# Performance work log

Hardware: AMD Instinct MI355X
Metric: run time of the kernel (lower is better)

Reference implementation:

```python
import jax, jax.numpy as jnp
import numpy as np

B, S, SR, H, NH, L, V, FF = 4, 512, 512, 1024, 16, 6, 32000, 4096
HD = H // NH  # 64
PAD = 2


def setup_inputs() -> dict:
    key = jax.random.key(0)
    ks = jax.random.split(key, 40)
    f32 = jnp.float32

    def n(k, shape, scale=0.02):
        return jax.random.normal(k, shape, f32) * scale

    encoder_outputs = jax.random.normal(ks[0], (B, SR, H), f32)
    decoder_input = jax.random.randint(ks[1], (B, S), 0, V)
    decoder_input = jnp.where(decoder_input == PAD, 3, decoder_input)
    decoder_input = decoder_input.at[:, S - 64:].set(PAD).at[:, 0].set(5)
    encoder_input = jax.random.randint(ks[2], (B, SR), 0, V)
    encoder_input = jnp.where(encoder_input == PAD, 3, encoder_input)
    encoder_input = encoder_input.at[:, SR - 64:].set(PAD)

    emb = jax.random.normal(ks[3], (V, H), f32).at[PAD].set(0.0)  # padding_idx=2 row is zero

    return {
        'encoder_outputs': encoder_outputs,
        'decoder_input': decoder_input,
        'encoder_input': encoder_input,
        'emb': emb,
        'wq1': n(ks[4], (L, H, H)), 'bq1': jnp.zeros((L, H), f32),
        'wk1': n(ks[5], (L, H, H)), 'bk1': jnp.zeros((L, H), f32),
        'wv1': n(ks[6], (L, H, H)), 'bv1': jnp.zeros((L, H), f32),
        'wo1': n(ks[7], (L, H, H)), 'bo1': jnp.zeros((L, H), f32),
        'pos1': jax.random.normal(ks[8], (L, 2 * S - 1, HD), f32),  # torch.randn init
        'wq2': n(ks[9], (L, H, H)), 'bq2': jnp.zeros((L, H), f32),
        'wk2': n(ks[10], (L, H, H)), 'bk2': jnp.zeros((L, H), f32),
        'wv2': n(ks[11], (L, H, H)), 'bv2': jnp.zeros((L, H), f32),
        'wo2': n(ks[12], (L, H, H)), 'bo2': jnp.zeros((L, H), f32),
        'ln1g': jnp.ones((L, H), f32), 'ln1b': jnp.zeros((L, H), f32),
        'ln2g': jnp.ones((L, H), f32), 'ln2b': jnp.zeros((L, H), f32),
        'ln3g': jnp.ones((L, H), f32), 'ln3b': jnp.zeros((L, H), f32),
        'wf1': n(ks[13], (L, H, FF)), 'bf1': jnp.zeros((L, FF), f32),
        'wf2': n(ks[14], (L, FF, H)), 'bf2': jnp.zeros((L, H), f32),
        'wout': n(ks[15], (H, V)), 'bout': jnp.zeros((V,), f32),
    }


def _split_heads(x):
    b, l, _ = x.shape
    return x.reshape(b, l, NH, HD).transpose(0, 2, 1, 3)  # b h l d


def _layer_norm(x, g, b):
    m = x.mean(-1, keepdims=True)
    v = ((x - m) ** 2).mean(-1, keepdims=True)
    return (x - m) / jnp.sqrt(v + 1e-5) * g + b


def _skew(q, P):
    # Transformer-XL style relative-position skew. q: [b,h,S,d] (already scaled), P: [2S-1,d]
    b = q.shape[0]
    pe = jnp.einsum('bhid,jd->bhij', q, P)                 # [b,h,S,2S-1]
    pe = jnp.pad(pe, ((0, 0), (0, 0), (0, 0), (0, 1)))      # [b,h,S,2S]
    pe = pe.reshape(b, NH, 2 * S * S)
    pe = jnp.pad(pe, ((0, 0), (0, 0), (0, S - 1)))
    pe = pe.reshape(b, NH, S + 1, 2 * S - 1)
    return pe[:, :, :-1, -S:]                               # [b,h,S,S]


def _attention(xq, xkv, wq, bq, wk, bk, wv, bv, wo, bo, pos, add_mask, causal):
    b = xq.shape[0]
    q = _split_heads(xq @ wq + bq) / np.float32(np.sqrt(HD))
    k = _split_heads(xkv @ wk + bk)
    v = _split_heads(xkv @ wv + bv)
    att = jnp.einsum('bhid,bhjd->bhij', q, k)
    if pos is not None:
        att = att + _skew(q, pos)
    if causal:
        i = jnp.arange(S)[:, None]
        j = jnp.arange(att.shape[-1])[None, :]
        att = jnp.where(j > i, -jnp.inf, att)
    if add_mask is not None:
        att = att + add_mask
    s = jax.nn.softmax(att, axis=-1)
    o = jnp.einsum('bhqk,bhkd->bhqd', s, v)
    o = o.transpose(0, 2, 1, 3).reshape(b, S, H)
    return o @ wo + bo


def _forward(encoder_outputs, decoder_input, encoder_input, emb,
             wq1, bq1, wk1, bk1, wv1, bv1, wo1, bo1, pos1,
             wq2, bq2, wk2, bk2, wv2, bv2, wo2, bo2,
             ln1g, ln1b, ln2g, ln2b, ln3g, ln3b,
             wf1, bf1, wf2, bf2, wout, bout):
    self_mask = jnp.where(decoder_input == PAD, -jnp.inf, 0.0)[:, None, None, :]   # [b,1,1,S]
    cross_mask = jnp.where(encoder_input == PAD, -jnp.inf, 0.0)[:, None, None, :]  # [b,1,1,SR]
    x = emb[decoder_input]  # dropout_p=0 -> identity
    for i in range(L):
        a1 = _attention(x, x, wq1[i], bq1[i], wk1[i], bk1[i], wv1[i], bv1[i],
                        wo1[i], bo1[i], pos1[i], self_mask, True)
        x1 = _layer_norm(a1 + x, ln1g[i], ln1b[i])
        a2 = _attention(x1, encoder_outputs, wq2[i], bq2[i], wk2[i], bk2[i], wv2[i], bv2[i],
                        wo2[i], bo2[i], None, cross_mask, False)
        x2 = _layer_norm(a2 + x1, ln2g[i], ln2b[i])
        ff = jax.nn.relu(x2 @ wf1[i] + bf1[i]) @ wf2[i] + bf2[i]
        x = _layer_norm(ff + x2, ln3g[i], ln3b[i])
    return jax.nn.log_softmax(x @ wout + bout, axis=-1)  # [b,S,V]


def reference(encoder_outputs, decoder_input, encoder_input, emb,
              wq1, bq1, wk1, bk1, wv1, bv1, wo1, bo1, pos1,
              wq2, bq2, wk2, bk2, wv2, bv2, wo2, bo2,
              ln1g, ln1b, ln2g, ln2b, ln3g, ln3b,
              wf1, bf1, wf2, bf2, wout, bout):
    return _forward(encoder_outputs, decoder_input, encoder_input, emb,
                    wq1, bq1, wk1, bk1, wv1, bv1, wo1, bo1, pos1,
                    wq2, bq2, wk2, bk2, wv2, bv2, wo2, bo2,
                    ln1g, ln1b, ln2g, ln2b, ln3g, ln3b,
                    wf1, bf1, wf2, bf2, wout, bout)
```

## Files before the change

kernel.cpp:

```cpp
#include <hip/hip_runtime.h>


typedef unsigned short u16;
typedef short s16x8 __attribute__((ext_vector_type(8)));
typedef unsigned short u16x4 __attribute__((ext_vector_type(4)));
typedef unsigned short u16x8 __attribute__((ext_vector_type(8)));
typedef float f32x4 __attribute__((ext_vector_type(4)));

#define PADTOK 2
#define NEG_INF (-__builtin_inff())

static __device__ __forceinline__ u16 f2bf(float f) {
  unsigned u = __float_as_uint(f);
  u += 0x7fffu + ((u >> 16) & 1u);
  return (u16)(u >> 16);
}
static __device__ __forceinline__ float bf2f(u16 h) {
  return __uint_as_float(((unsigned)h) << 16);
}
static __device__ __forceinline__ float f16tof(u16 h) {
  _Float16 x = __builtin_bit_cast(_Float16, h);
  return (float)x;
}
static __device__ __forceinline__ u16 ftof16(float v) {
  _Float16 x = (_Float16)v;
  return __builtin_bit_cast(u16, x);
}
static __device__ __forceinline__ f32x4 mfma16(s16x8 a, s16x8 b, f32x4 c) {
  asm("v_mfma_f32_16x16x32_bf16 %0, %1, %2, %0" : "+v"(c) : "v"(a), "v"(b));
  return c;
}
static __device__ __forceinline__ void gll16(const void* g, void* l) {
  __builtin_amdgcn_global_load_lds((const __attribute__((address_space(1))) void*)g,
                                   (__attribute__((address_space(3))) void*)l, 16, 0, 0);
}
static __device__ __forceinline__ size_t hsidx(int m, int n) {
  return ((size_t)((m >> 9) * 16 + (n >> 6))) * 32768u + (size_t)(m & 511) * 64u + (size_t)(n & 63);
}
static __device__ __forceinline__ size_t vtidx(int m, int n) {
  return ((size_t)((m >> 9) * 16 + (n >> 6))) * 65536u + (size_t)(n & 63) * 512u + (size_t)(m & 511);
}

static __device__ __forceinline__ void raster2(int& bm, int& bn, int GM0) {
  const int nm = gridDim.y, nn = gridDim.x;
  int bid = blockIdx.y * nn + blockIdx.x;
  const int nwg = nm * nn;
  const int q = nwg >> 3, r = nwg & 7;
  const int x = bid & 7, p = bid >> 3;
  bid = (x < r ? x * (q + 1) : r * (q + 1) + (x - r) * q) + p;
  const int GM = nm < GM0 ? nm : GM0;
  const int pg = GM * nn;
  const int gi = bid / pg, rem = bid - gi * pg;
  const int left = nm - gi * GM;
  const int gm = left < GM ? left : GM;
  bm = gi * GM + rem % gm;
  bn = rem / gm;
}

template<int EPI, bool BF16OUT, int MFR, bool RELU, bool RESID, int SKIP, int GMT>
__global__ __launch_bounds__(256)
void bgemm(const u16* __restrict__ A, long long sAg,
           const u16* __restrict__ Bt, long long sBg,
           const float* __restrict__ bias, const float* __restrict__ bias2,
           const float* __restrict__ bias3,
           const float* __restrict__ Res,
           void* __restrict__ Cv, u16* __restrict__ C2, u16* __restrict__ C3,
           long long sCg, int ldc, int K, float scale)
{
  constexpr int BM = MFR * 32;
  __shared__ u16 As[BM * 64];
  __shared__ u16 Bs[128 * 64];
  int bmi, bni;
  raster2(bmi, bni, GMT);
  const int bm0 = bmi * BM, bn0 = bni * 128;
  if constexpr (SKIP == 1) {
    if (bn0 > bm0 + BM - 1) return;
  }
  if constexpr (SKIP == 2) {
    if ((bm0 & 511) + bn0 <= 256) return;
  }
  const int g = blockIdx.z;
  const u16* Ag = A + (size_t)g * (size_t)sAg;
  const u16* Bg = Bt + (size_t)g * (size_t)sBg;
  const int tid = threadIdx.x, l = tid & 63, w = tid >> 6;
  const int wm = w >> 1, wn = w & 1;
  const int rsel = l & 15, kg = l >> 4, xs = l & 7;

  f32x4 acc[MFR][4];
#pragma unroll
  for (int i = 0; i < MFR; ++i)
#pragma unroll
    for (int j = 0; j < 4; ++j) acc[i][j] = (f32x4){0.f, 0.f, 0.f, 0.f};

  const int srow = l >> 3;
  const int sch  = (l & 7) ^ srow;
  const u16* Agp = Ag + ((size_t)(bm0 + w * 8 * MFR + srow)) * (size_t)K + sch * 8;
  const u16* Bgp = Bg + ((size_t)(bn0 + w * 32 + srow)) * (size_t)K + sch * 8;
  char* AsL = (char*)As + (w * 8 * MFR) * 128;
  char* BsL = (char*)Bs + (w * 32) * 128;

  for (int k0 = 0; k0 < K; k0 += 64) {
    __syncthreads();
#pragma unroll
    for (int i = 0; i < MFR; ++i)
      gll16(Agp + (size_t)i * 8 * K + k0, AsL + i * 1024);
#pragma unroll
    for (int i = 0; i < 4; ++i)
      gll16(Bgp + (size_t)i * 8 * K + k0, BsL + i * 1024);
    __syncthreads();

    const int arow0 = (wm * (MFR * 16) + rsel) * 128;
    const int brow0 = (wn * 64 + rsel) * 128;
#pragma unroll
    for (int ks = 0; ks < 2; ++ks) {
      const int ch = ((ks * 4 + kg) ^ xs) * 16;
      s16x8 af[MFR], bfr[4];
#pragma unroll
      for (int mf = 0; mf < MFR; ++mf)
        af[mf] = *(const s16x8*)((const char*)As + arow0 + mf * 2048 + ch);
#pragma unroll
      for (int nf = 0; nf < 4; ++nf)
        bfr[nf] = *(const s16x8*)((const char*)Bs + brow0 + nf * 2048 + ch);
#pragma unroll
      for (int mf = 0; mf < MFR; ++mf)
#pragma unroll
        for (int nf = 0; nf < 4; ++nf)
          acc[mf][nf] = mfma16(af[mf], bfr[nf], acc[mf][nf]);
    }
  }

#pragma unroll
  for (int mf = 0; mf < MFR; ++mf) {
#pragma unroll
    for (int nf = 0; nf < 4; ++nf) {
      const int n = bn0 + wn * 64 + nf * 16 + rsel;
      int sub = 0, nl = n;
      const float* bp = bias;
      if constexpr (EPI == 4) {
        sub = n >> 10; nl = n & 1023;
        bp = (sub == 0) ? bias : (sub == 1) ? bias2 : bias3;
      }
      if constexpr (EPI == 5) {
        sub = n >> 10; nl = n & 1023;
        bp = (sub == 0) ? bias : bias2;
      }
      const float bv = bp ? bp[nl] : 0.f;
      float sc = 1.f;
      if constexpr (EPI == 0 || EPI == 1) sc = scale;
      if constexpr (EPI == 4) sc = (sub == 0) ? scale : 1.f;
#pragma unroll
      for (int e = 0; e < 4; ++e) {
        const int m = bm0 + wm * (MFR * 16) + mf * 16 + kg * 4 + e;
        float v = (acc[mf][nf][e] + bv) * sc;
        if constexpr (RELU) v = fmaxf(v, 0.f);
        if constexpr (RESID) v += Res[(size_t)m * (size_t)ldc + n];
        if constexpr (EPI == 0) {
          const size_t idx = (size_t)g * (size_t)sCg + (size_t)m * (size_t)ldc + n;
          if constexpr (BF16OUT) ((u16*)Cv)[idx] = f2bf(v);
          else                   ((float*)Cv)[idx] = v;
        } else if constexpr (EPI == 1) {
          ((u16*)Cv)[hsidx(m, nl)] = f2bf(v);
        } else if constexpr (EPI == 4) {
          if (sub == 2)      C3[vtidx(m, nl)] = f2bf(v);
          else if (sub == 1) C2[hsidx(m, nl)] = f2bf(v);
          else               ((u16*)Cv)[hsidx(m, nl)] = f2bf(v);
        } else if constexpr (EPI == 5) {
          if (sub == 0) ((u16*)Cv)[hsidx(m, nl)] = f2bf(v);
          else          C2[vtidx(m, nl)] = f2bf(v);
        } else if constexpr (EPI == 6) {
          ((u16*)Cv)[(size_t)m * (size_t)ldc + n] = ftof16(v);
        }
      }
    }
  }
}

template<bool SELF>
__global__ __launch_bounds__(256)
void fused_attn(const u16* __restrict__ Qb, const u16* __restrict__ Kb,
                const u16* __restrict__ Vt, const u16* __restrict__ PE,
                const float* __restrict__ maskf, u16* __restrict__ O)
{
  __shared__ u16 SP[32][520];
  __shared__ float Of[4][32][68];
  __shared__ float rs[32];
  const int it = blockIdx.x, g = blockIdx.y, b = g >> 4, h = g & 15;
  const int i0 = it * 32;
  const int CT = SELF ? (i0 + 32) : 512;
  const int tid = threadIdx.x, l = tid & 63, w = tid >> 6;
  const int rsel = l & 15, kg = l >> 4;

  const u16* Qg = Qb + (size_t)g * 32768u;
  const u16* Kg = Kb + (size_t)g * 32768u;
  const u16* Vg = Vt + (size_t)g * 65536u;

  s16x8 qf[2][2];
#pragma unroll
  for (int rt = 0; rt < 2; ++rt)
#pragma unroll
    for (int ks = 0; ks < 2; ++ks)
      qf[rt][ks] = *(const s16x8*)(Qg + (size_t)(i0 + rt * 16 + rsel) * 64u + ks * 32 + kg * 8);

  for (int ct = w; ct * 16 < CT; ct += 4) {
    const int j = ct * 16 + rsel;
    const s16x8 kf0 = *(const s16x8*)(Kg + (size_t)j * 64u + kg * 8);
    const s16x8 kf1 = *(const s16x8*)(Kg + (size_t)j * 64u + 32 + kg * 8);
    f32x4 a0 = {0.f, 0.f, 0.f, 0.f}, a1 = {0.f, 0.f, 0.f, 0.f};
    a0 = mfma16(qf[0][0], kf0, a0);
    a0 = mfma16(qf[0][1], kf1, a0);
    a1 = mfma16(qf[1][0], kf0, a1);
    a1 = mfma16(qf[1][1], kf1, a1);
    const float mj = maskf[b * 512 + j];
#pragma unroll
    for (int rt = 0; rt < 2; ++rt) {
      const f32x4 av = rt ? a1 : a0;
#pragma unroll
      for (int e = 0; e < 4; ++e) {
        const int r = rt * 16 + kg * 4 + e;
        float v = av[e] + mj;
        if constexpr (SELF) {
          const int i = i0 + r;
          if (j > i) v = NEG_INF;
          else       v += bf2f(PE[((size_t)(g * 512 + i)) * 512u + (511 + j - i)]);
        }
        SP[r][j] = f2bf(v);
      }
    }
  }
  __syncthreads();

  const int r = tid >> 3, sc0 = (tid & 7) * 4;
  float mx = NEG_INF;
  for (int c = sc0; c < CT; c += 32) {
    const u16x4 h4 = *(const u16x4*)&SP[r][c];
#pragma unroll
    for (int e = 0; e < 4; ++e) mx = fmaxf(mx, bf2f(h4[e]));
  }
#pragma unroll
  for (int o = 1; o < 8; o <<= 1) mx = fmaxf(mx, __shfl_xor(mx, o, 64));
  float sum = 0.f;
  for (int c = sc0; c < CT; c += 32) {
    const u16x4 h4 = *(const u16x4*)&SP[r][c];
    const float p0 = expf(bf2f(h4[0]) - mx), p1 = expf(bf2f(h4[1]) - mx);
    const float p2 = expf(bf2f(h4[2]) - mx), p3 = expf(bf2f(h4[3]) - mx);
    sum += p0 + p1 + p2 + p3;
    const u16x4 o4 = {f2bf(p0), f2bf(p1), f2bf(p2), f2bf(p3)};
    *(u16x4*)&SP[r][c] = o4;
  }
#pragma unroll
  for (int o = 1; o < 8; o <<= 1) sum += __shfl_xor(sum, o, 64);
  if ((tid & 7) == 0) rs[r] = 1.f / sum;
  __syncthreads();

  f32x4 oa[2][4];
#pragma unroll
  for (int rt = 0; rt < 2; ++rt)
#pragma unroll
    for (int nt = 0; nt < 4; ++nt) oa[rt][nt] = (f32x4){0.f, 0.f, 0.f, 0.f};
  const int nk = CT >> 5;
  for (int kt = w; kt < nk; kt += 4) {
    const s16x8 pf0 = *(const s16x8*)&SP[rsel][kt * 32 + kg * 8];
    const s16x8 pf1 = *(const s16x8*)&SP[16 + rsel][kt * 32 + kg * 8];
    s16x8 vf[4];
#pragma unroll
    for (int nt = 0; nt < 4; ++nt)
      vf[nt] = *(const s16x8*)(Vg + (size_t)(nt * 16 + rsel) * 512u + kt * 32 + kg * 8);
#pragma unroll
    for (int nt = 0; nt < 4; ++nt) {
      oa[0][nt] = mfma16(pf0, vf[nt], oa[0][nt]);
      oa[1][nt] = mfma16(pf1, vf[nt], oa[1][nt]);
    }
  }
#pragma unroll
  for (int rt = 0; rt < 2; ++rt)
#pragma unroll
    for (int nt = 0; nt < 4; ++nt)
#pragma unroll
      for (int e = 0; e < 4; ++e)
        Of[w][rt * 16 + kg * 4 + e][nt * 16 + rsel] = oa[rt][nt][e];
  __syncthreads();

  const int c0 = (tid & 7) * 8;
  const float inv = rs[r];
  float ov[8];
#pragma unroll
  for (int q = 0; q < 2; ++q) {
    const float4 s0 = *(const float4*)&Of[0][r][c0 + q * 4];
    const float4 s1 = *(const float4*)&Of[1][r][c0 + q * 4];
    const float4 s2 = *(const float4*)&Of[2][r][c0 + q * 4];
    const float4 s3 = *(const float4*)&Of[3][r][c0 + q * 4];
    ov[q * 4 + 0] = (s0.x + s1.x + s2.x + s3.x) * inv;
    ov[q * 4 + 1] = (s0.y + s1.y + s2.y + s3.y) * inv;
    ov[q * 4 + 2] = (s0.z + s1.z + s2.z + s3.z) * inv;
    ov[q * 4 + 3] = (s0.w + s1.w + s2.w + s3.w) * inv;
  }
  const u16x8 o8 = {f2bf(ov[0]), f2bf(ov[1]), f2bf(ov[2]), f2bf(ov[3]),
                    f2bf(ov[4]), f2bf(ov[5]), f2bf(ov[6]), f2bf(ov[7])};
  *(u16x8*)(O + ((size_t)(b * 512 + i0 + r)) * 1024u + h * 64 + c0) = o8;
}

static __device__ __forceinline__ void tconv_tile(const float* in, int N,
                                                  u16* out, int K, int k0, int n0) {
  __shared__ u16 L[64][72];
  const int t = threadIdx.x;
  const int rk = t >> 4, cn = (t & 15) * 4;
#pragma unroll
  for (int q = 0; q < 4; ++q) {
    const int kk = k0 + rk + q * 16;
    float4 v = *(const float4*)(in + (size_t)kk * (size_t)N + n0 + cn);
    L[cn + 0][rk + q * 16] = f2bf(v.x);
    L[cn + 1][rk + q * 16] = f2bf(v.y);
    L[cn + 2][rk + q * 16] = f2bf(v.z);
    L[cn + 3][rk + q * 16] = f2bf(v.w);
  }
  __syncthreads();
  const int rn = t >> 2, ck = (t & 3) * 16;
  u16* op = out + (size_t)(n0 + rn) * (size_t)K + k0 + ck;
  *(s16x8*)op       = *(const s16x8*)&L[rn][ck];
  *(s16x8*)(op + 8) = *(const s16x8*)&L[rn][ck + 8];
}

__global__ __launch_bounds__(256)
void conv_layer(const float* w0, const float* w1, const float* w2, const float* w3,
                const float* w4, const float* w5, const float* w6, const float* w7,
                const float* w8, const float* w9, u16* WT) {
  const int b = blockIdx.x;
  const float* in; u16* out; int N, K, kt, nt;
  if (b < 2048) {
    const int j = b >> 8, t = b & 255;
    const float* ws[8] = {w0, w1, w2, w3, w4, w5, w6, w7};
    in = ws[j]; out = WT + (size_t)j * 1048576u; K = 1024; N = 1024;
    kt = t >> 4; nt = t & 15;
  } else if (b < 3072) {
    const int t = b - 2048;
    in = w8; out = WT + 8388608u; K = 1024; N = 4096; kt = t >> 6; nt = t & 63;
  } else {
    const int t = b - 3072;
    in = w9; out = WT + 12582912u; K = 4096; N = 1024; kt = t >> 4; nt = t & 15;
  }
  tconv_tile(in, N, out, K, kt * 64, nt * 64);
}

__global__ __launch_bounds__(256)
void conv_wout(const float* in, u16* out) {
  const int b = blockIdx.x;
  const int kt = b / 500, nt = b % 500;
  tconv_tile(in, 32000, out, 1024, kt * 64, nt * 64);
}

__global__ void conv_bf16(const float* __restrict__ in, u16* __restrict__ out) {
  const int i = (blockIdx.x * 256 + threadIdx.x) * 4;
  float4 v = *(const float4*)(in + i);
  u16x4 h = {f2bf(v.x), f2bf(v.y), f2bf(v.z), f2bf(v.w)};
  *(u16x4*)(out + i) = h;
}

__global__ void conv_pos(const float* __restrict__ pos, u16* __restrict__ posb) {
  const int idx = (blockIdx.x * 256 + threadIdx.x) * 4;
  const int lyr = idx >> 15, rem = idx & 32767;
  float4 v = *(const float4*)(pos + (size_t)lyr * 65472u + rem);
  u16x4 h = {f2bf(v.x), f2bf(v.y), f2bf(v.z), f2bf(v.w)};
  *(u16x4*)(posb + idx) = h;
}

__global__ void mask_kernel(const int* __restrict__ dec, const int* __restrict__ enc,
                            float* __restrict__ mD, float* __restrict__ mE) {
  const int i = blockIdx.x * 256 + threadIdx.x;
  mD[i] = (dec[i] == PADTOK) ? NEG_INF : 0.f;
  mE[i] = (enc[i] == PADTOK) ? NEG_INF : 0.f;
}

static __device__ __forceinline__ float wred_sum(float v) {
#pragma unroll
  for (int o = 32; o > 0; o >>= 1) v += __shfl_down(v, o, 64);
  return v;
}
static __device__ __forceinline__ float wred_max(float v) {
#pragma unroll
  for (int o = 32; o > 0; o >>= 1) v = fmaxf(v, __shfl_down(v, o, 64));
  return v;
}
static __device__ __forceinline__ float bred_sum(float v, float* sm) {
  const int lane = threadIdx.x & 63, wid = threadIdx.x >> 6;
  v = wred_sum(v);
  if (lane == 0) sm[wid] = v;
  __syncthreads();
  if (threadIdx.x == 0) sm[0] = sm[0] + sm[1] + sm[2] + sm[3];
  __syncthreads();
  const float r = sm[0];
  __syncthreads();
  return r;
}

__global__ void embed_kernel(const int* __restrict__ dec, const float* __restrict__ emb,
                             float* __restrict__ X, u16* __restrict__ Xh) {
  const int m = blockIdx.x, t = threadIdx.x;
  const int tok = dec[m];
  float4 v = ((const float4*)(emb + (size_t)tok * 1024u))[t];
  ((float4*)(X + (size_t)m * 1024u))[t] = v;
  u16x4 h = {f2bf(v.x), f2bf(v.y), f2bf(v.z), f2bf(v.w)};
  *(u16x4*)(Xh + (size_t)m * 1024u + t * 4) = h;
}

__global__ void layernorm_kernel(const float* __restrict__ R,
                                 const float* __restrict__ gw, const float* __restrict__ bw,
                                 float* __restrict__ Y, u16* __restrict__ Yh) {
  __shared__ float sm[4];
  const int m = blockIdx.x, t = threadIdx.x;
  float4 v = ((const float4*)(R + (size_t)m * 1024u))[t];
  float s = v.x + v.y + v.z + v.w;
  s = bred_sum(s, sm);
  const float mean = s * (1.f / 1024.f);
  const float d0 = v.x - mean, d1 = v.y - mean, d2 = v.z - mean, d3 = v.w - mean;
  float q = d0 * d0 + d1 * d1 + d2 * d2 + d3 * d3;
  q = bred_sum(q, sm);
  const float rstd = rsqrtf(q * (1.f / 1024.f) + 1e-5f);
  const int c = t * 4;
  float4 o;
  o.x = d0 * rstd * gw[c + 0] + bw[c + 0];
  o.y = d1 * rstd * gw[c + 1] + bw[c + 1];
  o.z = d2 * rstd * gw[c + 2] + bw[c + 2];
  o.w = d3 * rstd * gw[c + 3] + bw[c + 3];
  ((float4*)(Y + (size_t)m * 1024u))[t] = o;
  u16x4 h = {f2bf(o.x), f2bf(o.y), f2bf(o.z), f2bf(o.w)};
  *(u16x4*)(Yh + (size_t)m * 1024u + c) = h;
}

__global__ __launch_bounds__(512)
void log_softmax_kernel(float* __restrict__ out) {
  __shared__ u16 row[32000];
  __shared__ float sm[8];
  const int m = blockIdx.x, tid = threadIdx.x;
  const u16* src = (const u16*)out + (size_t)m * 64000u;
  for (int c = tid; c < 4000; c += 512)
    *(u16x8*)&row[c * 8] = *(const u16x8*)(src + c * 8);
  __syncthreads();
  float mx = NEG_INF;
  for (int c = tid; c < 4000; c += 512) {
    const u16x8 h = *(const u16x8*)&row[c * 8];
#pragma unroll
    for (int e = 0; e < 8; ++e) mx = fmaxf(mx, f16tof(h[e]));
  }
  mx = wred_max(mx);
  if ((tid & 63) == 0) sm[tid >> 6] = mx;
  __syncthreads();
  if (tid == 0) {
    float a = sm[0];
#pragma unroll
    for (int wI = 1; wI < 8; ++wI) a = fmaxf(a, sm[wI]);
    sm[0] = a;
  }
  __syncthreads();
  mx = sm[0];
  __syncthreads();
  float s = 0.f;
  for (int c = tid; c < 4000; c += 512) {
    const u16x8 h = *(const u16x8*)&row[c * 8];
#pragma unroll
    for (int e = 0; e < 8; ++e) s += expf(f16tof(h[e]) - mx);
  }
  s = wred_sum(s);
  if ((tid & 63) == 0) sm[tid >> 6] = s;
  __syncthreads();
  if (tid == 0) {
    float a = 0.f;
#pragma unroll
    for (int wI = 0; wI < 8; ++wI) a += sm[wI];
    sm[0] = a;
  }
  __syncthreads();
  const float lse = mx + logf(sm[0]);
  float* dst = out + (size_t)m * 32000u;
  for (int c = tid; c < 4000; c += 512) {
    const u16x8 h = *(const u16x8*)&row[c * 8];
    float4 o0, o1;
    o0.x = f16tof(h[0]) - lse; o0.y = f16tof(h[1]) - lse;
    o0.z = f16tof(h[2]) - lse; o0.w = f16tof(h[3]) - lse;
    o1.x = f16tof(h[4]) - lse; o1.y = f16tof(h[5]) - lse;
    o1.z = f16tof(h[6]) - lse; o1.w = f16tof(h[7]) - lse;
    ((float4*)dst)[c * 2]     = o0;
    ((float4*)dst)[c * 2 + 1] = o1;
  }
}

extern "C" void kernel_launch(void* const* d_in, const int* in_sizes, int n_in,
                              void* d_out, int out_size, void* d_ws, size_t ws_size,
                              hipStream_t stream) {
  const float* enc_out = (const float*)d_in[0];
  const int*   dec_in  = (const int*)d_in[1];
  const int*   enc_in  = (const int*)d_in[2];
  const float* emb     = (const float*)d_in[3];
  const float* wq1 = (const float*)d_in[4];  const float* bq1 = (const float*)d_in[5];
  const float* wk1 = (const float*)d_in[6];  const float* bk1 = (const float*)d_in[7];
  const float* wv1 = (const float*)d_in[8];  const float* bv1 = (const float*)d_in[9];
  const float* wo1 = (const float*)d_in[10]; const float* bo1 = (const float*)d_in[11];
  const float* pos1 = (const float*)d_in[12];
  const float* wq2 = (const float*)d_in[13]; const float* bq2 = (const float*)d_in[14];
  const float* wk2 = (const float*)d_in[15]; const float* bk2 = (const float*)d_in[16];
  const float* wv2 = (const float*)d_in[17]; const float* bv2 = (const float*)d_in[18];
  const float* wo2 = (const float*)d_in[19]; const float* bo2 = (const float*)d_in[20];
  const float* ln1g = (const float*)d_in[21]; const float* ln1b = (const float*)d_in[22];
  const float* ln2g = (const float*)d_in[23]; const float* ln2b = (const float*)d_in[24];
  const float* ln3g = (const float*)d_in[25]; const float* ln3b = (const float*)d_in[26];
  const float* wf1 = (const float*)d_in[27]; const float* bf1 = (const float*)d_in[28];
  const float* wf2 = (const float*)d_in[29]; const float* bf2 = (const float*)d_in[30];
  const float* wout = (const float*)d_in[31]; const float* bout = (const float*)d_in[32];

  char* ws = (char*)d_ws;
  u16*   WT    = (u16*)(ws + 0);
  float* maskD = (float*)(ws + 33554432);
  float* maskE = (float*)(ws + 33562624);
  u16*   WoutT = (u16*)(ws + 0);
  u16*   PEP   = (u16*)(ws + 67108864);
  float* X     = (float*)(ws + 100663296);
  float* Xa    = (float*)(ws + 109051904);
  float* Xb    = (float*)(ws + 117440512);
  float* Rb    = (float*)(ws + 125829120);
  u16*   Ab16  = (u16*)(ws + 134217728);
  u16*   Q     = (u16*)(ws + 138412032);
  u16*   Kh    = (u16*)(ws + 142606336);
  u16*   VT    = (u16*)(ws + 146800640);
  u16*   Ob16  = (u16*)(ws + 155189248);
  u16*   FFH16 = (u16*)(ws + 159383552);
  u16*   encb  = (u16*)(ws + 176160768);
  u16*   posb  = (u16*)(ws + 180355072);
  float* out   = (float*)d_out;

  embed_kernel<<<2048, 256, 0, stream>>>(dec_in, emb, X, Ab16);
  conv_bf16<<<2048, 256, 0, stream>>>(enc_out, encb);
  conv_pos<<<192, 256, 0, stream>>>(pos1, posb);
  mask_kernel<<<8, 256, 0, stream>>>(dec_in, enc_in, maskD, maskE);

  for (int i = 0; i < 6; ++i) {
    const size_t oHH = (size_t)i * 1048576u, oH = (size_t)i * 1024u;
    const float* bq1i = bq1 + oH; const float* bk1i = bk1 + oH;
    const float* bv1i = bv1 + oH; const float* bo1i = bo1 + oH;
    const float* bq2i = bq2 + oH; const float* bk2i = bk2 + oH;
    const float* bv2i = bv2 + oH; const float* bo2i = bo2 + oH;
    const float* bf1i = bf1 + (size_t)i * 4096u; const float* bf2i = bf2 + oH;
    const u16* posL = posb + (size_t)i * 32768u;

    conv_layer<<<4096, 256, 0, stream>>>(
        wq1 + oHH, wk1 + oHH, wv1 + oHH, wo1 + oHH,
        wq2 + oHH, wk2 + oHH, wv2 + oHH, wo2 + oHH,
        wf1 + (size_t)i * 4194304u, wf2 + (size_t)i * 4194304u, WT);

    bgemm<4, true, 4, false, false, 0, 8><<<dim3(24, 16, 1), 256, 0, stream>>>(
        Ab16, 0, WT, 0, bq1i, bk1i, bv1i, nullptr, Q, Kh, VT, 0, 0, 1024, 0.125f);
    bgemm<0, true, 4, false, false, 2, 8><<<dim3(4, 256, 1), 256, 0, stream>>>(
        Q, 0, posL, 0, nullptr, nullptr, nullptr, nullptr, PEP, nullptr, nullptr,
        0, 512, 64, 1.f);
    fused_attn<true><<<dim3(16, 64), 256, 0, stream>>>(Q, Kh, VT, PEP, maskD, Ob16);
    bgemm<0, false, 2, false, true, 0, 8><<<dim3(8, 32, 1), 256, 0, stream>>>(
        Ob16, 0, WT + 3145728u, 0, bo1i, nullptr, nullptr, X, Rb, nullptr, nullptr,
        0, 1024, 1024, 1.f);
    layernorm_kernel<<<2048, 256, 0, stream>>>(Rb, ln1g + oH, ln1b + oH, Xa, Ab16);

    bgemm<1, true, 2, false, false, 0, 8><<<dim3(8, 32, 1), 256, 0, stream>>>(
        Ab16, 0, WT + 4194304u, 0, bq2i, nullptr, nullptr, nullptr, Q, nullptr, nullptr,
        0, 0, 1024, 0.125f);
    bgemm<5, true, 4, false, false, 0, 8><<<dim3(16, 16, 1), 256, 0, stream>>>(
        encb, 0, WT + 5242880u, 0, bk2i, bv2i, nullptr, nullptr, Kh, VT, nullptr,
        0, 0, 1024, 1.f);
    fused_attn<false><<<dim3(16, 64), 256, 0, stream>>>(Q, Kh, VT, nullptr, maskE, Ob16);
    bgemm<0, false, 2, false, true, 0, 8><<<dim3(8, 32, 1), 256, 0, stream>>>(
        Ob16, 0, WT + 7340032u, 0, bo2i, nullptr, nullptr, Xa, Rb, nullptr, nullptr,
        0, 1024, 1024, 1.f);
    layernorm_kernel<<<2048, 256, 0, stream>>>(Rb, ln2g + oH, ln2b + oH, Xb, Ab16);

    bgemm<0, true, 4, true, false, 0, 8><<<dim3(32, 16, 1), 256, 0, stream>>>(
        Ab16, 0, WT + 8388608u, 0, bf1i, nullptr, nullptr, nullptr, FFH16, nullptr, nullptr,
        0, 4096, 1024, 1.f);
    bgemm<0, false, 2, false, true, 0, 8><<<dim3(8, 32, 1), 256, 0, stream>>>(
        FFH16, 0, WT + 12582912u, 0, bf2i, nullptr, nullptr, Xb, Rb, nullptr, nullptr,
        0, 1024, 4096, 1.f);
    layernorm_kernel<<<2048, 256, 0, stream>>>(Rb, ln3g + oH, ln3b + oH, X, Ab16);
  }

  conv_wout<<<8000, 256, 0, stream>>>(wout, WoutT);
  bgemm<6, false, 4, false, false, 0, 16><<<dim3(250, 16, 1), 256, 0, stream>>>(
      Ab16, 0, WoutT, 0, bout, nullptr, nullptr, nullptr, out, nullptr, nullptr,
      0, 64000, 1024, 1.f);
  log_softmax_kernel<<<2048, 512, 0, stream>>>(out);
}
```

Before: 2.311 ms.

## Give each attention wave its own 16-row query tile and drop block barriers

```diff
diff --git a/kernel.cpp b/kernel.cpp
--- a/kernel.cpp
+++ b/kernel.cpp
@@ -73,9 +73,6 @@
   int bmi, bni;
   raster2(bmi, bni, GMT);
   const int bm0 = bmi * BM, bn0 = bni * 128;
-  if constexpr (SKIP == 1) {
-    if (bn0 > bm0 + BM - 1) return;
-  }
   if constexpr (SKIP == 2) {
     if ((bm0 & 511) + bn0 <= 256) return;
   }
@@ -181,122 +178,98 @@
                 const u16* __restrict__ Vt, const u16* __restrict__ PE,
                 const float* __restrict__ maskf, u16* __restrict__ O)
 {
-  __shared__ u16 SP[32][520];
-  __shared__ float Of[4][32][68];
-  __shared__ float rs[32];
-  const int it = blockIdx.x, g = blockIdx.y, b = g >> 4, h = g & 15;
-  const int i0 = it * 32;
-  const int CT = SELF ? (i0 + 32) : 512;
+  __shared__ u16 SP[4][16][520];
+  __shared__ float rsm[4][16];
+  const int bid = blockIdx.y * 8 + blockIdx.x;
+  const int g = (bid & 7) + 8 * ((bid >> 3) & 7);
+  const int rt = bid >> 6;
+  const int b = g >> 4, h = g & 15;
   const int tid = threadIdx.x, l = tid & 63, w = tid >> 6;
+  const int ti = SELF ? (w * 8 + rt) : (rt * 4 + w);
+  const int i0 = ti * 16;
+  const int CT = SELF ? (i0 + 16) : 512;
   const int rsel = l & 15, kg = l >> 4;
 
   const u16* Qg = Qb + (size_t)g * 32768u;
   const u16* Kg = Kb + (size_t)g * 32768u;
   const u16* Vg = Vt + (size_t)g * 65536u;
-
-  s16x8 qf[2][2];
-#pragma unroll
-  for (int rt = 0; rt < 2; ++rt)
-#pragma unroll
-    for (int ks = 0; ks < 2; ++ks)
-      qf[rt][ks] = *(const s16x8*)(Qg + (size_t)(i0 + rt * 16 + rsel) * 64u + ks * 32 + kg * 8);
-
-  for (int ct = w; ct * 16 < CT; ct += 4) {
-    const int j = ct * 16 + rsel;
-    const s16x8 kf0 = *(const s16x8*)(Kg + (size_t)j * 64u + kg * 8);
-    const s16x8 kf1 = *(const s16x8*)(Kg + (size_t)j * 64u + 32 + kg * 8);
-    f32x4 a0 = {0.f, 0.f, 0.f, 0.f}, a1 = {0.f, 0.f, 0.f, 0.f};
-    a0 = mfma16(qf[0][0], kf0, a0);
-    a0 = mfma16(qf[0][1], kf1, a0);
-    a1 = mfma16(qf[1][0], kf0, a1);
-    a1 = mfma16(qf[1][1], kf1, a1);
-    const float mj = maskf[b * 512 + j];
-#pragma unroll
-    for (int rt = 0; rt < 2; ++rt) {
-      const f32x4 av = rt ? a1 : a0;
-#pragma unroll
-      for (int e = 0; e < 4; ++e) {
-        const int r = rt * 16 + kg * 4 + e;
-        float v = av[e] + mj;
-        if constexpr (SELF) {
-          const int i = i0 + r;
-          if (j > i) v = NEG_INF;
-          else       v += bf2f(PE[((size_t)(g * 512 + i)) * 512u + (511 + j - i)]);
-        }
-        SP[r][j] = f2bf(v);
+  u16 (*sp)[520] = SP[w];
+  float* rs = rsm[w];
+
+  const s16x8 qf0 = *(const s16x8*)(Qg + (size_t)(i0 + rsel) * 64u + kg * 8);
+  const s16x8 qf1 = *(const s16x8*)(Qg + (size_t)(i0 + rsel) * 64u + 32 + kg * 8);
+
+  for (int j0 = 0; j0 < CT; j0 += 16) {
+    const s16x8 kf0 = *(const s16x8*)(Kg + (size_t)(j0 + rsel) * 64u + kg * 8);
+    const s16x8 kf1 = *(const s16x8*)(Kg + (size_t)(j0 + rsel) * 64u + 32 + kg * 8);
+    f32x4 a = {0.f, 0.f, 0.f, 0.f};
+    a = mfma16(qf0, kf0, a);
+    a = mfma16(qf1, kf1, a);
+    const int jj = j0 + rsel;
+    const float mj = maskf[b * 512 + jj];
+#pragma unroll
+    for (int e = 0; e < 4; ++e) {
+      const int r = kg * 4 + e;
+      float v = a[e] + mj;
+      if constexpr (SELF) {
+        const int i = i0 + r;
+        if (jj > i) v = NEG_INF;
+        else        v += bf2f(PE[((size_t)(g * 512 + i)) * 512u + (511 + jj - i)]);
       }
+      sp[r][jj] = f2bf(v);
     }
   }
-  __syncthreads();
-
-  const int r = tid >> 3, sc0 = (tid & 7) * 4;
+  asm volatile("s_waitcnt lgkmcnt(0)" ::: "memory");
+
+  const int sr = l >> 2, sub = l & 3;
   float mx = NEG_INF;
-  for (int c = sc0; c < CT; c += 32) {
-    const u16x4 h4 = *(const u16x4*)&SP[r][c];
+  for (int c = sub * 4; c < CT; c += 16) {
+    const u16x4 h4 = *(const u16x4*)&sp[sr][c];
 #pragma unroll
     for (int e = 0; e < 4; ++e) mx = fmaxf(mx, bf2f(h4[e]));
   }
-#pragma unroll
-  for (int o = 1; o < 8; o <<= 1) mx = fmaxf(mx, __shfl_xor(mx, o, 64));
+  mx = fmaxf(mx, __shfl_xor(mx, 1, 64));
+  mx = fmaxf(mx, __shfl_xor(mx, 2, 64));
   float sum = 0.f;
-  for (int c = sc0; c < CT; c += 32) {
-    const u16x4 h4 = *(const u16x4*)&SP[r][c];
+  for (int c = sub * 4; c < CT; c += 16) {
+    const u16x4 h4 = *(const u16x4*)&sp[sr][c];
     const float p0 = expf(bf2f(h4[0]) - mx), p1 = expf(bf2f(h4[1]) - mx);
     const float p2 = expf(bf2f(h4[2]) - mx), p3 = expf(bf2f(h4[3]) - mx);
     sum += p0 + p1 + p2 + p3;
     const u16x4 o4 = {f2bf(p0), f2bf(p1), f2bf(p2), f2bf(p3)};
-    *(u16x4*)&SP[r][c] = o4;
-  }
-#pragma unroll
-  for (int o = 1; o < 8; o <<= 1) sum += __shfl_xor(sum, o, 64);
-  if ((tid & 7) == 0) rs[r] = 1.f / sum;
-  __syncthreads();
-
-  f32x4 oa[2][4];
-#pragma unroll
-  for (int rt = 0; rt < 2; ++rt)
-#pragma unroll
-    for (int nt = 0; nt < 4; ++nt) oa[rt][nt] = (f32x4){0.f, 0.f, 0.f, 0.f};
-  const int nk = CT >> 5;
-  for (int kt = w; kt < nk; kt += 4) {
-    const s16x8 pf0 = *(const s16x8*)&SP[rsel][kt * 32 + kg * 8];
-    const s16x8 pf1 = *(const s16x8*)&SP[16 + rsel][kt * 32 + kg * 8];
-    s16x8 vf[4];
+    *(u16x4*)&sp[sr][c] = o4;
+  }
+  sum += __shfl_xor(sum, 1, 64);
+  sum += __shfl_xor(sum, 2, 64);
+  if (sub == 0) rs[sr] = 1.f / sum;
+  if (CT & 31) {
+    const u16x4 z = {0, 0, 0, 0};
+    *(u16x4*)&sp[sr][CT + sub * 4] = z;
+  }
+  asm volatile("s_waitcnt lgkmcnt(0)" ::: "memory");
+
+  f32x4 oa[4];
+#pragma unroll
+  for (int nt = 0; nt < 4; ++nt) oa[nt] = (f32x4){0.f, 0.f, 0.f, 0.f};
+  const int nk = (CT + 31) >> 5;
+  for (int kt = 0; kt < nk; ++kt) {
+    const s16x8 pf = *(const s16x8*)&sp[rsel][kt * 32 + kg * 8];
+#pragma unroll
+    for (int nt = 0; nt < 4; ++nt) {
+      const s16x8 vf = *(const s16x8*)(Vg + (size_t)(nt * 16 + rsel) * 512u + kt * 32 + kg * 8);
+      oa[nt] = mfma16(pf, vf, oa[nt]);
+    }
+  }
+
+#pragma unroll
+  for (int e = 0; e < 4; ++e) {
+    const int q = kg * 4 + e;
+    const float inv = rs[q];
+    u16* orow = O + ((size_t)(b * 512 + i0 + q)) * 1024u + h * 64;
 #pragma unroll
     for (int nt = 0; nt < 4; ++nt)
-      vf[nt] = *(const s16x8*)(Vg + (size_t)(nt * 16 + rsel) * 512u + kt * 32 + kg * 8);
-#pragma unroll
-    for (int nt = 0; nt < 4; ++nt) {
-      oa[0][nt] = mfma16(pf0, vf[nt], oa[0][nt]);
-      oa[1][nt] = mfma16(pf1, vf[nt], oa[1][nt]);
-    }
-  }
-#pragma unroll
-  for (int rt = 0; rt < 2; ++rt)
-#pragma unroll
-    for (int nt = 0; nt < 4; ++nt)
-#pragma unroll
-      for (int e = 0; e < 4; ++e)
-        Of[w][rt * 16 + kg * 4 + e][nt * 16 + rsel] = oa[rt][nt][e];
-  __syncthreads();
-
-  const int c0 = (tid & 7) * 8;
-  const float inv = rs[r];
-  float ov[8];
-#pragma unroll
-  for (int q = 0; q < 2; ++q) {
-    const float4 s0 = *(const float4*)&Of[0][r][c0 + q * 4];
-    const float4 s1 = *(const float4*)&Of[1][r][c0 + q * 4];
-    const float4 s2 = *(const float4*)&Of[2][r][c0 + q * 4];
-    const float4 s3 = *(const float4*)&Of[3][r][c0 + q * 4];
-    ov[q * 4 + 0] = (s0.x + s1.x + s2.x + s3.x) * inv;
-    ov[q * 4 + 1] = (s0.y + s1.y + s2.y + s3.y) * inv;
-    ov[q * 4 + 2] = (s0.z + s1.z + s2.z + s3.z) * inv;
-    ov[q * 4 + 3] = (s0.w + s1.w + s2.w + s3.w) * inv;
-  }
-  const u16x8 o8 = {f2bf(ov[0]), f2bf(ov[1]), f2bf(ov[2]), f2bf(ov[3]),
-                    f2bf(ov[4]), f2bf(ov[5]), f2bf(ov[6]), f2bf(ov[7])};
-  *(u16x8*)(O + ((size_t)(b * 512 + i0 + r)) * 1024u + h * 64 + c0) = o8;
+      orow[nt * 16 + rsel] = f2bf(oa[nt][e] * inv);
+  }
 }
 
 static __device__ __forceinline__ void tconv_tile(const float* in, int N,
@@ -550,7 +523,7 @@
     bgemm<0, true, 4, false, false, 2, 8><<<dim3(4, 256, 1), 256, 0, stream>>>(
         Q, 0, posL, 0, nullptr, nullptr, nullptr, nullptr, PEP, nullptr, nullptr,
         0, 512, 64, 1.f);
-    fused_attn<true><<<dim3(16, 64), 256, 0, stream>>>(Q, Kh, VT, PEP, maskD, Ob16);
+    fused_attn<true><<<dim3(8, 64), 256, 0, stream>>>(Q, Kh, VT, PEP, maskD, Ob16);
     bgemm<0, false, 2, false, true, 0, 8><<<dim3(8, 32, 1), 256, 0, stream>>>(
         Ob16, 0, WT + 3145728u, 0, bo1i, nullptr, nullptr, X, Rb, nullptr, nullptr,
         0, 1024, 1024, 1.f);
@@ -562,7 +535,7 @@
     bgemm<5, true, 4, false, false, 0, 8><<<dim3(16, 16, 1), 256, 0, stream>>>(
         encb, 0, WT + 5242880u, 0, bk2i, bv2i, nullptr, nullptr, Kh, VT, nullptr,
         0, 0, 1024, 1.f);
-    fused_attn<false><<<dim3(16, 64), 256, 0, stream>>>(Q, Kh, VT, nullptr, maskE, Ob16);
+    fused_attn<false><<<dim3(8, 64), 256, 0, stream>>>(Q, Kh, VT, nullptr, maskE, Ob16);
     bgemm<0, false, 2, false, true, 0, 8><<<dim3(8, 32, 1), 256, 0, stream>>>(
         Ob16, 0, WT + 7340032u, 0, bo2i, nullptr, nullptr, Xa, Rb, nullptr, nullptr,
         0, 1024, 1024, 1.f);
```

New measurement: 2.270 ms. Within noise of the previous version (-1.8%).
